# Kernel tuning notes

Hardware: AMD Instinct MI355X
Metric: run time of the kernel (lower is better)

The kernel has to match this reference:

```python
import jax, jax.numpy as jnp
import numpy as np

N_NODES = 100000
N_EDGES = 1600000
F_IN = 128
HID = 128  # nhid*2
NHID = 64
N_GRAPHS = 512
N_CLASSES = 10
NEG_SLOPE = 0.2  # PyG GATConv default


def setup_inputs() -> dict:
    key = jax.random.key(0)
    ks = jax.random.split(key, 16)
    x = jax.random.normal(ks[0], (N_NODES, F_IN), dtype=jnp.float32)
    edge_index = jax.random.randint(ks[1], (2, N_EDGES), 0, N_NODES, dtype=jnp.int64)
    batch = jnp.sort(jax.random.randint(ks[2], (N_NODES,), 0, N_GRAPHS, dtype=jnp.int64))
    def lin(k, fan_in, shape):
        bound = 1.0 / np.sqrt(fan_in)
        return jax.random.uniform(k, shape, jnp.float32, -bound, bound)
    return {
        "x": x, "edge_index": edge_index, "batch": batch,
        "W1": lin(ks[3], F_IN, (F_IN, HID)),
        "a_src1": lin(ks[4], HID, (HID,)),
        "a_dst1": lin(ks[5], HID, (HID,)),
        "b1": jnp.zeros((HID,), jnp.float32),
        "W2": lin(ks[6], HID, (HID, HID)),
        "a_src2": lin(ks[7], HID, (HID,)),
        "a_dst2": lin(ks[8], HID, (HID,)),
        "b2": jnp.zeros((HID,), jnp.float32),
        "W_fc1": lin(ks[9], HID, (HID, NHID)),
        "b_fc1": lin(ks[10], HID, (NHID,)),
        "W_fc2": lin(ks[11], NHID, (NHID, N_CLASSES)),
        "b_fc2": lin(ks[12], NHID, (N_CLASSES,)),
    }


def gat_conv(x, src, dst, W, a_src, a_dst, b):
    # h = W x ; attention e_ij = LeakyReLU(a_src.h_i + a_dst.h_j), softmax over
    # incoming edges of each destination j, then scatter-add aggregation.
    h = x @ W                                   # [N, H]
    alpha_s = h @ a_src                         # [N]
    alpha_d = h @ a_dst                         # [N]
    e = jax.nn.leaky_relu(alpha_s[src] + alpha_d[dst], NEG_SLOPE)  # [E]
    n = x.shape[0]
    m = jax.ops.segment_max(e, dst, num_segments=n)                # per-dst max
    ex = jnp.exp(e - m[dst])
    denom = jax.ops.segment_sum(ex, dst, num_segments=n)
    alpha = ex / denom[dst]                                        # [E]
    out = jax.ops.segment_sum(alpha[:, None] * h[src], dst, num_segments=n)
    return out + b


def reference(x, edge_index, batch, W1, a_src1, a_dst1, b1,
              W2, a_src2, a_dst2, b2, W_fc1, b_fc1, W_fc2, b_fc2):
    n = x.shape[0]
    # GATConv default add_self_loops=True
    loops = jnp.arange(n, dtype=edge_index.dtype)
    src = jnp.concatenate([edge_index[0], loops])
    dst = jnp.concatenate([edge_index[1], loops])

    h = jax.nn.selu(gat_conv(x, src, dst, W1, a_src1, a_dst1, b1))
    h = jax.nn.selu(gat_conv(h, src, dst, W2, a_src2, a_dst2, b2))

    # global mean pool over graphs
    sums = jax.ops.segment_sum(h, batch, num_segments=N_GRAPHS)
    cnts = jax.ops.segment_sum(jnp.ones((n,), h.dtype), batch, num_segments=N_GRAPHS)
    pooled = jax.nn.selu(sums / jnp.maximum(cnts, 1.0)[:, None])   # [G, H]

    g = jax.nn.selu(pooled @ W_fc1 + b_fc1)
    # dropout p=0.5 is identity in eval mode
    logits = g @ W_fc2 + b_fc2
    return jax.nn.log_softmax(logits, axis=-1)
```

## Files before the change

### kernel.cpp

```cpp
#include <hip/hip_runtime.h>
#include <hip/hip_bf16.h>

#define NEG_SLOPE 0.2f
typedef unsigned int uint32;

#define BSHIFT 9
#define BSIZE 512
#define MAXB 256
#define PCHUNK 2048
#define PEPT 8
#define BSTRIDE 12288

typedef __attribute__((ext_vector_type(8))) __bf16 bf16x8;
typedef __attribute__((ext_vector_type(4))) float f32x4;
typedef __attribute__((ext_vector_type(2))) float f32x2;

__device__ __forceinline__ float selu_f(float x) {
    const float a = 1.6732632423543772f, s = 1.0507009873554805f;
    return x > 0.0f ? s * x : s * a * (__expf(x) - 1.0f);
}

__device__ __forceinline__ unsigned short f2bf(float x) {
    uint32 u = __float_as_uint(x);
    uint32 r = (u + 0x7fff + ((u >> 16) & 1)) >> 16;
    return (unsigned short)r;
}
__device__ __forceinline__ float bf_lo(uint32 g) { return __uint_as_float(g << 16); }
__device__ __forceinline__ float bf_hi(uint32 g) { return __uint_as_float(g & 0xffff0000u); }

__global__ __launch_bounds__(256) void prep9(const float* __restrict__ W1,
                                             const float* __restrict__ W2,
                                             unsigned short* __restrict__ Wb,
                                             const int* __restrict__ batch,
                                             int* __restrict__ gstart,
                                             int N, int G) {
    int b = blockIdx.x, t = threadIdx.x;
    if (b < 2) {
        const float* W = b ? W2 : W1;
        unsigned short* oh = Wb + (size_t)b * 32768;
        unsigned short* ol = oh + 16384;
        for (int d = t; d < 16384; d += 256) {
            int j = d & 7, nn = (d >> 3) & 127, g = d >> 10;
            float v = W[(g * 8 + j) * 128 + nn];
            uint32 hu = f2bf(v);
            float hv = __uint_as_float(hu << 16);
            oh[d] = (unsigned short)hu;
            ol[d] = f2bf(v - hv);
        }
    } else {
        int i = (b - 2) * 256 + t;
        if (i < N) {
            int bb = batch[i];
            int bp = (i == 0) ? -1 : batch[i - 1];
            for (int q = bp + 1; q <= bb; ++q) gstart[q] = i;
            if (i == N - 1)
                for (int q = bb + 1; q <= G; ++q) gstart[q] = N;
        }
    }
}

__global__ __launch_bounds__(256) void partition_edges(const int* __restrict__ ei,
                                                       int* __restrict__ gcur0,
                                                       uint32* __restrict__ tmp,
                                                       int E, int TOT) {
    __shared__ int lcnt[MAXB];
    __shared__ int lstart[MAXB];
    __shared__ int lcur[MAXB];
    __shared__ int gbase[MAXB];
    __shared__ uint32 staged[PCHUNK];
    __shared__ unsigned char bslot[PCHUNK];
    int t = threadIdx.x;
    int eb = blockIdx.x * PCHUNK;
    int sreg[PEPT], dreg[PEPT];
    #pragma unroll
    for (int k = 0; k < PEPT; ++k) {
        int e = eb + k * 256 + t;
        if (e < TOT) {
            if (e < E) { sreg[k] = ei[e]; dreg[k] = ei[E + e]; }
            else       { sreg[k] = dreg[k] = e - E; }
        } else dreg[k] = -1;
    }
    lcnt[t] = 0;
    __syncthreads();
    #pragma unroll
    for (int k = 0; k < PEPT; ++k)
        if (dreg[k] >= 0) atomicAdd(&lcnt[dreg[k] >> BSHIFT], 1);
    __syncthreads();
    int v = lcnt[t];
    lstart[t] = v;
    __syncthreads();
    for (int off = 1; off < 256; off <<= 1) {
        int add = (t >= off) ? lstart[t - off] : 0;
        __syncthreads();
        lstart[t] += add;
        __syncthreads();
    }
    int ex = lstart[t] - v;
    __syncthreads();
    lstart[t] = ex;
    lcur[t] = ex;
    if (v > 0) gbase[t] = t * BSTRIDE + atomicAdd(&gcur0[t], v);
    __syncthreads();
    #pragma unroll
    for (int k = 0; k < PEPT; ++k) {
        int d = dreg[k];
        if (d >= 0) {
            int b = d >> BSHIFT;
            int p = atomicAdd(&lcur[b], 1);
            staged[p] = ((uint32)(d & (BSIZE - 1)) << 17) | (uint32)sreg[k];
            bslot[p] = (unsigned char)b;
        }
    }
    __syncthreads();
    int nvalid = TOT - eb; if (nvalid > PCHUNK) nvalid = PCHUNK;
    for (int i = t; i < nvalid; i += 256) {
        int b = bslot[i];
        tmp[gbase[b] + (i - lstart[b])] = staged[i];
    }
}

__global__ __launch_bounds__(1024) void bucket_build(const uint32* __restrict__ tmp,
                                                     const int* __restrict__ gcur0,
                                                     int* __restrict__ rowptr,
                                                     int* __restrict__ rowend,
                                                     int* __restrict__ col,
                                                     int N, int NB) {
    __shared__ int cnt[BSIZE];
    __shared__ int sums[256];
    int b = blockIdx.x, t = threadIdx.x;
    int lo = b << BSHIFT;
    int nn = N - lo; if (nn > BSIZE) nn = BSIZE;
    if (t < BSIZE) cnt[t] = 0;
    __syncthreads();
    int ebeg = b * BSTRIDE;
    int eend = ebeg + gcur0[b];
    for (int i = ebeg + t; i < eend; i += 1024)
        atomicAdd(&cnt[tmp[i] >> 17], 1);
    __syncthreads();
    int c0 = 0, c1 = 0, s2 = 0;
    if (t < 256) {
        c0 = cnt[2 * t]; c1 = cnt[2 * t + 1];
        s2 = c0 + c1;
        sums[t] = s2;
    }
    __syncthreads();
    for (int off = 1; off < 256; off <<= 1) {
        int add = (t < 256 && t >= off) ? sums[t - off] : 0;
        __syncthreads();
        if (t < 256) sums[t] += add;
        __syncthreads();
    }
    if (t < 256) {
        int ex = sums[t] - s2;
        int st0 = ebeg + ex, st1 = st0 + c0;
        if (2 * t < nn)     { rowptr[lo + 2 * t] = st0;     rowend[lo + 2 * t] = st0 + c0; }
        if (2 * t + 1 < nn) { rowptr[lo + 2 * t + 1] = st1; rowend[lo + 2 * t + 1] = st1 + c1; }
        cnt[2 * t] = st0; cnt[2 * t + 1] = st1;
    }
    __syncthreads();
    for (int i = ebeg + t; i < eend; i += 1024) {
        uint32 u = tmp[i];
        int p = atomicAdd(&cnt[u >> 17], 1);
        col[p] = (int)(u & 0x1FFFFu);
    }
}

__device__ __forceinline__ void gemm_core(const bf16x8 ah[2][4],
                                          const __bf16* Wl,
                                          const float* a_src, const float* a_dst,
                                          uint32* hb, float* as_, float* ad_,
                                          int rbase, int n, int col16, int quad) {
    f32x4 acc[2][8];
    #pragma unroll
    for (int mt = 0; mt < 2; ++mt)
        #pragma unroll
        for (int t = 0; t < 8; ++t) acc[mt][t] = (f32x4)(0.0f);

    #pragma unroll
    for (int c = 0; c < 4; ++c) {
        #pragma unroll
        for (int t = 0; t < 8; ++t) {
            int off = (((c * 4 + quad) * 128) + t * 16 + col16) * 8;
            bf16x8 bh = *(const bf16x8*)&Wl[off];
            bf16x8 bl = *(const bf16x8*)&Wl[16384 + off];
            #pragma unroll
            for (int mt = 0; mt < 2; ++mt) {
                acc[mt][t] = __builtin_amdgcn_mfma_f32_16x16x32_bf16(ah[mt][c], bh, acc[mt][t], 0, 0, 0);
                acc[mt][t] = __builtin_amdgcn_mfma_f32_16x16x32_bf16(ah[mt][c], bl, acc[mt][t], 0, 0, 0);
            }
        }
    }
    float asv[8], adv[8];
    #pragma unroll
    for (int t = 0; t < 8; ++t) { asv[t] = a_src[t * 16 + col16]; adv[t] = a_dst[t * 16 + col16]; }
    #pragma unroll
    for (int mt = 0; mt < 2; ++mt) {
        #pragma unroll
        for (int reg = 0; reg < 4; ++reg) {
            float s = 0.0f, d = 0.0f;
            #pragma unroll
            for (int t = 0; t < 8; ++t) {
                float v = acc[mt][t][reg];
                s += v * asv[t]; d += v * adv[t];
            }
            #pragma unroll
            for (int off = 1; off < 16; off <<= 1) {
                s += __shfl_xor(s, off);
                d += __shfl_xor(d, off);
            }
            int r = rbase + mt * 16 + quad * 4 + reg;
            if (col16 == 0 && r < n) { as_[r] = s; ad_[r] = d; }
        }
    }
    #pragma unroll
    for (int mt = 0; mt < 2; ++mt)
    #pragma unroll
    for (int t = 0; t < 8; ++t)
    #pragma unroll
    for (int reg = 0; reg < 4; ++reg) {
        float v = acc[mt][t][reg];
        float p = __shfl_xor(v, 1);
        int r = rbase + mt * 16 + quad * 4 + reg;
        if (!(col16 & 1) && r < n) {
            uint32 pk = (uint32)f2bf(v) | ((uint32)f2bf(p) << 16);
            hb[(size_t)r * 64 + t * 8 + (col16 >> 1)] = pk;
        }
    }
}

__global__ __launch_bounds__(256) void gemm_mfma_f32(const float* __restrict__ X,
                                                     const unsigned short* __restrict__ Wbh,
                                                     const float* __restrict__ a_src,
                                                     const float* __restrict__ a_dst,
                                                     uint32* __restrict__ hb,
                                                     float* __restrict__ as_,
                                                     float* __restrict__ ad_, int n) {
    __shared__ __bf16 Wl[32768];
    const int tid = threadIdx.x;
    {
        const uint4* sw = (const uint4*)Wbh;
        uint4* dw = (uint4*)Wl;
        for (int i = tid; i < 4096; i += 256) dw[i] = sw[i];
    }
    const int lane = tid & 63, wid = tid >> 6;
    const int col16 = lane & 15, quad = lane >> 4;
    const int rbase = blockIdx.x * 128 + wid * 32;
    bf16x8 ah[2][4];
    #pragma unroll
    for (int mt = 0; mt < 2; ++mt) {
        int r = rbase + mt * 16 + col16;
        bool ok = (r < n);
        const float* xp = X + (size_t)r * 128;
        #pragma unroll
        for (int c = 0; c < 4; ++c) {
            int k0 = c * 32 + quad * 8;
            float4 x0 = ok ? *(const float4*)(xp + k0)     : make_float4(0.f,0.f,0.f,0.f);
            float4 x1 = ok ? *(const float4*)(xp + k0 + 4) : make_float4(0.f,0.f,0.f,0.f);
            float xs[8] = {x0.x,x0.y,x0.z,x0.w,x1.x,x1.y,x1.z,x1.w};
            #pragma unroll
            for (int j = 0; j < 8; ++j) ah[mt][c][j] = (__bf16)xs[j];
        }
    }
    __syncthreads();
    gemm_core(ah, Wl, a_src, a_dst, hb, as_, ad_, rbase, n, col16, quad);
}

__global__ __launch_bounds__(256) void gemm_mfma_bf16(const __bf16* __restrict__ X,
                                                      const unsigned short* __restrict__ Wbh,
                                                      const float* __restrict__ a_src,
                                                      const float* __restrict__ a_dst,
                                                      uint32* __restrict__ hb,
                                                      float* __restrict__ as_,
                                                      float* __restrict__ ad_, int n) {
    __shared__ __bf16 Wl[32768];
    const int tid = threadIdx.x;
    {
        const uint4* sw = (const uint4*)Wbh;
        uint4* dw = (uint4*)Wl;
        for (int i = tid; i < 4096; i += 256) dw[i] = sw[i];
    }
    const int lane = tid & 63, wid = tid >> 6;
    const int col16 = lane & 15, quad = lane >> 4;
    const int rbase = blockIdx.x * 128 + wid * 32;
    bf16x8 ah[2][4];
    const bf16x8 zz = (bf16x8)((__bf16)0.0f);
    #pragma unroll
    for (int mt = 0; mt < 2; ++mt) {
        int r = rbase + mt * 16 + col16;
        bool ok = (r < n);
        const __bf16* xp = X + (size_t)r * 128;
        #pragma unroll
        for (int c = 0; c < 4; ++c)
            ah[mt][c] = ok ? *(const bf16x8*)(xp + c * 32 + quad * 8) : zz;
    }
    __syncthreads();
    gemm_core(ah, Wl, a_src, a_dst, hb, as_, ad_, rbase, n, col16, quad);
}

#define GIDX8(SARR, T0) { _Pragma("unroll") \
    for (int k_ = 0; k_ < 8; ++k_) { int t_ = (T0) + k_; \
        int sv_ = (t_ < 16) ? s0 : s1; \
        int si_ = __shfl(sv_, base + (t_ & 15)); \
        SARR[k_] = (t_ < cnt) ? si_ : 0; } }

#define GLOAD8(GARR, SARR) { _Pragma("unroll") \
    for (int k_ = 0; k_ < 8; ++k_) GARR[k_] = hb4[(uint32)SARR[k_] * 16u + l]; }

#define GW8(WARR, T0) { _Pragma("unroll") \
    for (int k_ = 0; k_ < 8; ++k_) { int t_ = (T0) + k_; \
        float wv_ = (t_ < 16) ? w0 : w1; \
        float wf_ = __shfl(wv_, base + (t_ & 15)); \
        WARR[k_] = (t_ < cnt) ? wf_ : 0.0f; } }

#define GCONSUME(GARR, WARR) { _Pragma("unroll") \
    for (int k_ = 0; k_ < 8; ++k_) { \
        f32x2 wv_ = (f32x2)WARR[k_]; \
        f32x2 u0_ = { bf_lo(GARR[k_].x), bf_hi(GARR[k_].x) }; \
        f32x2 u1_ = { bf_lo(GARR[k_].y), bf_hi(GARR[k_].y) }; \
        f32x2 u2_ = { bf_lo(GARR[k_].z), bf_hi(GARR[k_].z) }; \
        f32x2 u3_ = { bf_lo(GARR[k_].w), bf_hi(GARR[k_].w) }; \
        ac[0] = __builtin_elementwise_fma(wv_, u0_, ac[0]); \
        ac[1] = __builtin_elementwise_fma(wv_, u1_, ac[1]); \
        ac[2] = __builtin_elementwise_fma(wv_, u2_, ac[2]); \
        ac[3] = __builtin_elementwise_fma(wv_, u3_, ac[3]); } }

__global__ __launch_bounds__(256) void gat_csr5(const int* __restrict__ rowptr,
                                                const int* __restrict__ rowend,
                                                const int* __restrict__ col,
                                                const uint4* __restrict__ hb4,
                                                const float* __restrict__ as_,
                                                const float* __restrict__ ad_,
                                                const float* __restrict__ bias,
                                                uint4* __restrict__ outb, int n) {
    const int wid = threadIdx.x >> 6;
    const int lane = threadIdx.x & 63;
    const int q = lane >> 4, l = lane & 15;
    const int base = lane & 48;
    const int node = blockIdx.x * 16 + wid * 4 + q;
    const bool valid = node < n;
    int beg = 0, end = 0;
    if (valid) { beg = rowptr[node]; end = rowend[node]; }
    float add = valid ? ad_[node] : 0.0f;
    int deg = end - beg;
    int m1 = max(deg, __shfl_xor(deg, 16));
    int mdeg = max(m1, __shfl_xor(m1, 32));
    float s = 0.0f;
    f32x2 ac[4];
    #pragma unroll
    for (int p = 0; p < 4; ++p) ac[p] = (f32x2)(0.0f);

    for (int cb = 0; cb < mdeg; cb += 32) {
        int j0 = beg + cb + l, j1 = j0 + 16;
        bool e0 = (j0 < end), e1 = (j1 < end);
        int s0 = e0 ? col[j0] : 0;
        int s1 = e1 ? col[j1] : 0;
        int cnt = end - beg - cb;
        cnt = (cnt < 0) ? 0 : (cnt > 32 ? 32 : cnt);
        int rem = mdeg - cb; if (rem > 32) rem = 32;
        const int NB8 = (rem + 7) >> 3;

        int si[8]; uint4 gA[8], gB[8]; float wA[8], wB[8];

        GIDX8(si, 0); GLOAD8(gA, si);

        float v0 = as_[s0] + add;
        float v1 = as_[s1] + add;
        v0 = (v0 > 0.0f) ? v0 : NEG_SLOPE * v0;
        v1 = (v1 > 0.0f) ? v1 : NEG_SLOPE * v1;
        float w0 = e0 ? __expf(v0) : 0.0f;
        float w1 = e1 ? __expf(v1) : 0.0f;
        float ws = w0 + w1;
        #pragma unroll
        for (int off = 8; off > 0; off >>= 1) ws += __shfl_xor(ws, off);
        s += ws;
        GW8(wA, 0);

        int b = 0;
        while (true) {
            bool moreB = (b + 1 < NB8);
            if (moreB) { GIDX8(si, (b + 1) * 8); GLOAD8(gB, si); GW8(wB, (b + 1) * 8); }
            GCONSUME(gA, wA);
            if (!moreB) break;
            bool moreA = (b + 2 < NB8);
            if (moreA) { GIDX8(si, (b + 2) * 8); GLOAD8(gA, si); GW8(wA, (b + 2) * 8); }
            GCONSUME(gB, wB);
            if (!moreA) break;
            b += 2;
        }
    }
    if (valid) {
        float inv = 1.0f / s;
        float4 b0 = *(const float4*)&bias[l * 8];
        float4 b1 = *(const float4*)&bias[l * 8 + 4];
        float r0 = selu_f(ac[0].x * inv + b0.x);
        float r1 = selu_f(ac[0].y * inv + b0.y);
        float r2 = selu_f(ac[1].x * inv + b0.z);
        float r3 = selu_f(ac[1].y * inv + b0.w);
        float r4 = selu_f(ac[2].x * inv + b1.x);
        float r5 = selu_f(ac[2].y * inv + b1.y);
        float r6 = selu_f(ac[3].x * inv + b1.z);
        float r7 = selu_f(ac[3].y * inv + b1.w);
        uint4 o;
        o.x = (uint32)f2bf(r0) | ((uint32)f2bf(r1) << 16);
        o.y = (uint32)f2bf(r2) | ((uint32)f2bf(r3) << 16);
        o.z = (uint32)f2bf(r4) | ((uint32)f2bf(r5) << 16);
        o.w = (uint32)f2bf(r6) | ((uint32)f2bf(r7) << 16);
        outb[(uint32)node * 16u + l] = o;
    }
}

__global__ __launch_bounds__(128) void pool_head(const uint32* __restrict__ act,
                                                 const int* __restrict__ gstart,
                                                 const float* __restrict__ Wfc1,
                                                 const float* __restrict__ bfc1,
                                                 const float* __restrict__ Wfc2,
                                                 const float* __restrict__ bfc2,
                                                 float* __restrict__ out) {
    __shared__ float part[128][2];
    __shared__ float p[128];
    __shared__ float q[64];
    __shared__ float l[10];
    __shared__ float red[2];
    int g = blockIdx.x, t = threadIdx.x;
    int lo = gstart[g], hi = gstart[g + 1];
    int half = t >> 6, u = t & 63;
    float acc0 = 0.f, acc1 = 0.f;
    for (int nd = lo + half; nd < hi; nd += 2) {
        uint32 gv = act[(uint32)nd * 64u + u];
        acc0 += bf_lo(gv); acc1 += bf_hi(gv);
    }
    part[t][0] = acc0; part[t][1] = acc1;
    __syncthreads();
    if (half == 0) {
        float c = fmaxf((float)(hi - lo), 1.0f);
        p[2 * u]     = selu_f((acc0 + part[t + 64][0]) / c);
        p[2 * u + 1] = selu_f((acc1 + part[t + 64][1]) / c);
    }
    __syncthreads();
    if (t < 64) {
        float a = bfc1[t];
        #pragma unroll 8
        for (int k = 0; k < 128; ++k) a += p[k] * Wfc1[k * 64 + t];
        q[t] = selu_f(a);
    }
    __syncthreads();
    if (t < 10) {
        float a = bfc2[t];
        #pragma unroll
        for (int k = 0; k < 64; ++k) a += q[k] * Wfc2[k * 10 + t];
        l[t] = a;
    }
    __syncthreads();
    if (t == 0) {
        float mx = l[0];
        for (int c = 1; c < 10; ++c) mx = fmaxf(mx, l[c]);
        float sum = 0.0f;
        for (int c = 0; c < 10; ++c) sum += __expf(l[c] - mx);
        red[0] = mx; red[1] = logf(sum);
    }
    __syncthreads();
    if (t < 10) out[g * 10 + t] = l[t] - red[0] - red[1];
}

extern "C" void kernel_launch(void* const* d_in, const int* in_sizes, int n_in,
                              void* d_out, int out_size, void* d_ws, size_t ws_size,
                              hipStream_t stream) {
    const float* x      = (const float*)d_in[0];
    const int*   ei     = (const int*)d_in[1];
    const int*   batch  = (const int*)d_in[2];
    const float* W1     = (const float*)d_in[3];
    const float* asrc1  = (const float*)d_in[4];
    const float* adst1  = (const float*)d_in[5];
    const float* b1     = (const float*)d_in[6];
    const float* W2     = (const float*)d_in[7];
    const float* asrc2  = (const float*)d_in[8];
    const float* adst2  = (const float*)d_in[9];
    const float* b2     = (const float*)d_in[10];
    const float* Wfc1   = (const float*)d_in[11];
    const float* bfc1   = (const float*)d_in[12];
    const float* Wfc2   = (const float*)d_in[13];
    const float* bfc2   = (const float*)d_in[14];
    float* out = (float*)d_out;

    const int N = in_sizes[0] / 128;
    const int E = in_sizes[1] / 2;
    const int G = out_size / 10;
    const int TOT = E + N;
    const int NB = ((N - 1) >> BSHIFT) + 1;
    const int GB = (N + 255) / 256;
    const int PH = (TOT + PCHUNK - 1) / PCHUNK;
    const int GemmG = (N + 127) / 128;

    uint32* hb    = (uint32*)d_ws;
    uint32* h2b   = hb + (size_t)N * 64;
    uint32* tmp   = h2b + (size_t)N * 64;
    int*    col   = (int*)(tmp + (size_t)NB * BSTRIDE);
    float* as_    = (float*)(col + (size_t)NB * BSTRIDE);
    float* ad_    = as_ + N;
    int*   gstart = (int*)(ad_ + N);
    int*   rowptr = gstart + (G + 2);
    int*   rowend = rowptr + (N + 2);
    int*   gcur0  = rowend + (N + 2);
    unsigned short* Wb = (unsigned short*)(((uintptr_t)(gcur0 + MAXB) + 255) & ~(uintptr_t)255);

    const int gatGrid = (N + 15) / 16;

    hipMemsetAsync(gcur0, 0, MAXB * 4, stream);
    prep9<<<2 + GB, 256, 0, stream>>>(W1, W2, Wb, batch, gstart, N, G);
    partition_edges<<<PH, 256, 0, stream>>>(ei, gcur0, tmp, E, TOT);
    bucket_build<<<NB, 1024, 0, stream>>>(tmp, gcur0, rowptr, rowend, col, N, NB);

    gemm_mfma_f32<<<GemmG, 256, 0, stream>>>(x, Wb, asrc1, adst1, hb, as_, ad_, N);
    gat_csr5<<<gatGrid, 256, 0, stream>>>(rowptr, rowend, col, (const uint4*)hb, as_, ad_, b1, (uint4*)h2b, N);

    gemm_mfma_bf16<<<GemmG, 256, 0, stream>>>((const __bf16*)h2b, Wb + 32768, asrc2, adst2, hb, as_, ad_, N);
    gat_csr5<<<gatGrid, 256, 0, stream>>>(rowptr, rowend, col, (const uint4*)hb, as_, ad_, b2, (uint4*)h2b, N);

    pool_head<<<G, 128, 0, stream>>>(h2b, gstart, Wfc1, bfc1, Wfc2, bfc2, out);
}
```

Before: 398.8 us.

## Fuse mean-pool accumulation into second GAT layer and enlarge GEMM blocks

The second GAT aggregation kernel now atomically adds its SELU outputs into per-graph fp32 sums instead of writing bf16 node features, and the pool/head kernel just reads those sums. This removes the write and re-read of the full layer-2 activation tensor and the serial per-graph reduction. The cost is many float atomics into a small 512x128 buffer, which will contend heavily because batch is sorted and neighbouring nodes share a graph. Separately, the GEMM kernels switch to 512-thread blocks covering 256 rows, which amortises the shared-memory weight load over more rows.

```diff
diff --git a/kernel.cpp b/kernel.cpp
--- a/kernel.cpp
+++ b/kernel.cpp
@@ -228,7 +228,7 @@
     }
 }
 
-__global__ __launch_bounds__(256) void gemm_mfma_f32(const float* __restrict__ X,
+__global__ __launch_bounds__(512) void gemm_mfma_f32(const float* __restrict__ X,
                                                      const unsigned short* __restrict__ Wbh,
                                                      const float* __restrict__ a_src,
                                                      const float* __restrict__ a_dst,
@@ -240,11 +240,11 @@
     {
         const uint4* sw = (const uint4*)Wbh;
         uint4* dw = (uint4*)Wl;
-        for (int i = tid; i < 4096; i += 256) dw[i] = sw[i];
+        for (int i = tid; i < 4096; i += 512) dw[i] = sw[i];
     }
     const int lane = tid & 63, wid = tid >> 6;
     const int col16 = lane & 15, quad = lane >> 4;
-    const int rbase = blockIdx.x * 128 + wid * 32;
+    const int rbase = blockIdx.x * 256 + wid * 32;
     bf16x8 ah[2][4];
     #pragma unroll
     for (int mt = 0; mt < 2; ++mt) {
@@ -265,7 +265,7 @@
     gemm_core(ah, Wl, a_src, a_dst, hb, as_, ad_, rbase, n, col16, quad);
 }
 
-__global__ __launch_bounds__(256) void gemm_mfma_bf16(const __bf16* __restrict__ X,
+__global__ __launch_bounds__(512) void gemm_mfma_bf16(const __bf16* __restrict__ X,
                                                       const unsigned short* __restrict__ Wbh,
                                                       const float* __restrict__ a_src,
                                                       const float* __restrict__ a_dst,
@@ -277,11 +277,11 @@
     {
         const uint4* sw = (const uint4*)Wbh;
         uint4* dw = (uint4*)Wl;
-        for (int i = tid; i < 4096; i += 256) dw[i] = sw[i];
+        for (int i = tid; i < 4096; i += 512) dw[i] = sw[i];
     }
     const int lane = tid & 63, wid = tid >> 6;
     const int col16 = lane & 15, quad = lane >> 4;
-    const int rbase = blockIdx.x * 128 + wid * 32;
+    const int rbase = blockIdx.x * 256 + wid * 32;
     bf16x8 ah[2][4];
     const bf16x8 zz = (bf16x8)((__bf16)0.0f);
     #pragma unroll
@@ -324,14 +324,18 @@
         ac[2] = __builtin_elementwise_fma(wv_, u2_, ac[2]); \
         ac[3] = __builtin_elementwise_fma(wv_, u3_, ac[3]); } }
 
-__global__ __launch_bounds__(256) void gat_csr5(const int* __restrict__ rowptr,
+template<bool POOL>
+__global__ __launch_bounds__(256) void gat_csr6(const int* __restrict__ rowptr,
                                                 const int* __restrict__ rowend,
                                                 const int* __restrict__ col,
                                                 const uint4* __restrict__ hb4,
                                                 const float* __restrict__ as_,
                                                 const float* __restrict__ ad_,
                                                 const float* __restrict__ bias,
-                                                uint4* __restrict__ outb, int n) {
+                                                uint4* __restrict__ outb,
+                                                float* __restrict__ gsum,
+                                                const int* __restrict__ batch,
+                                                int n) {
     const int wid = threadIdx.x >> 6;
     const int lane = threadIdx.x & 63;
     const int q = lane >> 4, l = lane & 15;
@@ -400,42 +404,39 @@
         float r5 = selu_f(ac[2].y * inv + b1.y);
         float r6 = selu_f(ac[3].x * inv + b1.z);
         float r7 = selu_f(ac[3].y * inv + b1.w);
-        uint4 o;
-        o.x = (uint32)f2bf(r0) | ((uint32)f2bf(r1) << 16);
-        o.y = (uint32)f2bf(r2) | ((uint32)f2bf(r3) << 16);
-        o.z = (uint32)f2bf(r4) | ((uint32)f2bf(r5) << 16);
-        o.w = (uint32)f2bf(r6) | ((uint32)f2bf(r7) << 16);
-        outb[(uint32)node * 16u + l] = o;
-    }
-}
-
-__global__ __launch_bounds__(128) void pool_head(const uint32* __restrict__ act,
-                                                 const int* __restrict__ gstart,
-                                                 const float* __restrict__ Wfc1,
-                                                 const float* __restrict__ bfc1,
-                                                 const float* __restrict__ Wfc2,
-                                                 const float* __restrict__ bfc2,
-                                                 float* __restrict__ out) {
-    __shared__ float part[128][2];
+        if (POOL) {
+            int g = batch[node];
+            float* gp = gsum + (size_t)g * 128 + l * 8;
+            atomicAdd(gp + 0, r0); atomicAdd(gp + 1, r1);
+            atomicAdd(gp + 2, r2); atomicAdd(gp + 3, r3);
+            atomicAdd(gp + 4, r4); atomicAdd(gp + 5, r5);
+            atomicAdd(gp + 6, r6); atomicAdd(gp + 7, r7);
+        } else {
+            uint4 o;
+            o.x = (uint32)f2bf(r0) | ((uint32)f2bf(r1) << 16);
+            o.y = (uint32)f2bf(r2) | ((uint32)f2bf(r3) << 16);
+            o.z = (uint32)f2bf(r4) | ((uint32)f2bf(r5) << 16);
+            o.w = (uint32)f2bf(r6) | ((uint32)f2bf(r7) << 16);
+            outb[(uint32)node * 16u + l] = o;
+        }
+    }
+}
+
+__global__ __launch_bounds__(128) void pool_head2(const float* __restrict__ gsum,
+                                                  const int* __restrict__ gstart,
+                                                  const float* __restrict__ Wfc1,
+                                                  const float* __restrict__ bfc1,
+                                                  const float* __restrict__ Wfc2,
+                                                  const float* __restrict__ bfc2,
+                                                  float* __restrict__ out) {
     __shared__ float p[128];
     __shared__ float q[64];
     __shared__ float l[10];
     __shared__ float red[2];
     int g = blockIdx.x, t = threadIdx.x;
     int lo = gstart[g], hi = gstart[g + 1];
-    int half = t >> 6, u = t & 63;
-    float acc0 = 0.f, acc1 = 0.f;
-    for (int nd = lo + half; nd < hi; nd += 2) {
-        uint32 gv = act[(uint32)nd * 64u + u];
-        acc0 += bf_lo(gv); acc1 += bf_hi(gv);
-    }
-    part[t][0] = acc0; part[t][1] = acc1;
-    __syncthreads();
-    if (half == 0) {
-        float c = fmaxf((float)(hi - lo), 1.0f);
-        p[2 * u]     = selu_f((acc0 + part[t + 64][0]) / c);
-        p[2 * u + 1] = selu_f((acc1 + part[t + 64][1]) / c);
-    }
+    float c = fmaxf((float)(hi - lo), 1.0f);
+    p[t] = selu_f(gsum[(size_t)g * 128 + t] / c);
     __syncthreads();
     if (t < 64) {
         float a = bfc1[t];
@@ -453,9 +454,9 @@
     __syncthreads();
     if (t == 0) {
         float mx = l[0];
-        for (int c = 1; c < 10; ++c) mx = fmaxf(mx, l[c]);
+        for (int c2 = 1; c2 < 10; ++c2) mx = fmaxf(mx, l[c2]);
         float sum = 0.0f;
-        for (int c = 0; c < 10; ++c) sum += __expf(l[c] - mx);
+        for (int c2 = 0; c2 < 10; ++c2) sum += __expf(l[c2] - mx);
         red[0] = mx; red[1] = logf(sum);
     }
     __syncthreads();
@@ -489,7 +490,7 @@
     const int NB = ((N - 1) >> BSHIFT) + 1;
     const int GB = (N + 255) / 256;
     const int PH = (TOT + PCHUNK - 1) / PCHUNK;
-    const int GemmG = (N + 127) / 128;
+    const int GemmG = (N + 255) / 256;
 
     uint32* hb    = (uint32*)d_ws;
     uint32* h2b   = hb + (size_t)N * 64;
@@ -502,19 +503,23 @@
     int*   rowend = rowptr + (N + 2);
     int*   gcur0  = rowend + (N + 2);
     unsigned short* Wb = (unsigned short*)(((uintptr_t)(gcur0 + MAXB) + 255) & ~(uintptr_t)255);
+    float* gsum = (float*)(Wb + 2 * 32768);
 
     const int gatGrid = (N + 15) / 16;
 
     hipMemsetAsync(gcur0, 0, MAXB * 4, stream);
+    hipMemsetAsync(gsum, 0, (size_t)G * 128 * 4, stream);
     prep9<<<2 + GB, 256, 0, stream>>>(W1, W2, Wb, batch, gstart, N, G);
     partition_edges<<<PH, 256, 0, stream>>>(ei, gcur0, tmp, E, TOT);
     bucket_build<<<NB, 1024, 0, stream>>>(tmp, gcur0, rowptr, rowend, col, N, NB);
 
-    gemm_mfma_f32<<<GemmG, 256, 0, stream>>>(x, Wb, asrc1, adst1, hb, as_, ad_, N);
-    gat_csr5<<<gatGrid, 256, 0, stream>>>(rowptr, rowend, col, (const uint4*)hb, as_, ad_, b1, (uint4*)h2b, N);
-
-    gemm_mfma_bf16<<<GemmG, 256, 0, stream>>>((const __bf16*)h2b, Wb + 32768, asrc2, adst2, hb, as_, ad_, N);
-    gat_csr5<<<gatGrid, 256, 0, stream>>>(rowptr, rowend, col, (const uint4*)hb, as_, ad_, b2, (uint4*)h2b, N);
-
-    pool_head<<<G, 128, 0, stream>>>(h2b, gstart, Wfc1, bfc1, Wfc2, bfc2, out);
-}
+    gemm_mfma_f32<<<GemmG, 512, 0, stream>>>(x, Wb, asrc1, adst1, hb, as_, ad_, N);
+    gat_csr6<false><<<gatGrid, 256, 0, stream>>>(rowptr, rowend, col, (const uint4*)hb,
+                                                 as_, ad_, b1, (uint4*)h2b, nullptr, nullptr, N);
+
+    gemm_mfma_bf16<<<GemmG, 512, 0, stream>>>((const __bf16*)h2b, Wb + 32768, asrc2, adst2, hb, as_, ad_, N);
+    gat_csr6<true><<<gatGrid, 256, 0, stream>>>(rowptr, rowend, col, (const uint4*)hb,
+                                                as_, ad_, b2, nullptr, gsum, batch, N);
+
+    pool_head2<<<G, 128, 0, stream>>>(gsum, gstart, Wfc1, bfc1, Wfc2, bfc2, out);
+}
```

After: 900.2 us. +125.7%, slower.
